# Kernel tuning notes

Hardware: AMD Instinct MI355X
Metric: run time of the kernel (lower is better)

Reference implementation:

```python
import jax, jax.numpy as jnp
import numpy as np

N, H, W, DIM = 8, 32, 32, 768
HEAD_DIM = 64
NUM_HEADS = DIM // HEAD_DIM
KERNEL = (7, 7)
ROT_DIM = HEAD_DIM // 2  # 32
POS_DIM = 2
THETA = 10000.0
LN_EPS = 1e-5


def setup_inputs() -> dict:
    key = jax.random.key(0)
    k_x, k_qkv, k_out = jax.random.split(key, 3)
    S = H * W
    x = jax.random.normal(k_x, (N, S, DIM), dtype=jnp.float32)
    # 2D grid positions, same for every batch element
    grid = jnp.stack(jnp.meshgrid(jnp.arange(H), jnp.arange(W), indexing='ij'), axis=-1)
    pos = jnp.broadcast_to(grid.reshape(1, S, 2), (N, S, 2)).astype(jnp.int32)
    padding_mask = jnp.ones((N, S), dtype=bool)
    ln_g = jnp.ones((DIM,), dtype=jnp.float32)
    ln_b = jnp.zeros((DIM,), dtype=jnp.float32)
    w_qkv = jax.random.normal(k_qkv, (DIM, 3 * DIM), dtype=jnp.float32) * 0.02
    b_qkv = jnp.zeros((3 * DIM,), dtype=jnp.float32)
    w_out = jax.random.normal(k_out, (DIM, DIM), dtype=jnp.float32) * 0.02
    b_out = jnp.zeros((DIM,), dtype=jnp.float32)
    return {"x": x, "pos": pos, "padding_mask": padding_mask,
            "ln_g": ln_g, "ln_b": ln_b,
            "w_qkv": w_qkv, "b_qkv": b_qkv,
            "w_out": w_out, "b_out": b_out}


def _rope_cos_sin(pos):
    # freqs: theta ** linspace(0, -1, rot_dim // (pos_dim*2) + 1)[:-1] -> 8 freqs
    n_freq = ROT_DIM // (POS_DIM * 2)
    freqs = THETA ** jnp.linspace(0.0, -1.0, n_freq + 1, dtype=jnp.float32)[:-1]
    # pos: [n, s, 2] -> [n, s, 2, n_freq] -> [n, s, 2*n_freq] -> [n, 1, s, 2*n_freq]
    tmp = (pos[..., None].astype(jnp.float32) * freqs).reshape(*pos.shape[:-1], -1)[:, None]
    return jnp.cos(tmp), jnp.sin(tmp)


def _apply_rotary(x, cos, sin):
    d = cos.shape[-1]  # 16
    x1, x2, x3 = x[..., :d], x[..., d:2 * d], x[..., 2 * d:]
    y1 = x1 * cos - x2 * sin
    y2 = x2 * cos + x1 * sin
    return jnp.concatenate((y1.astype(x3.dtype), y2.astype(x3.dtype), x3), axis=-1)


def _attn_mask(pos, padding_mask, kernel_size):
    dh = pos[:, :, None, 0] - pos[:, None, :, 0]  # [n, s, s]
    dw = pos[:, :, None, 1] - pos[:, None, :, 1]
    kh, kw = kernel_size
    m = ((dh <= kh // 2) & (dh > -((kh + 1) // 2))
         & (dw <= kw // 2) & (dw > -((kw + 1) // 2)))
    m = m & (padding_mask[:, None, :] & padding_mask[:, :, None])
    return m[:, None]  # [n, 1, s, s]


def reference(x, pos, padding_mask, ln_g, ln_b, w_qkv, b_qkv, w_out, b_out):
    n, s, dim = x.shape
    skip = x
    # LayerNorm
    mu = jnp.mean(x, axis=-1, keepdims=True)
    var = jnp.mean(jnp.square(x - mu), axis=-1, keepdims=True)
    xn = (x - mu) * jax.lax.rsqrt(var + LN_EPS) * ln_g + ln_b
    # QKV projection; split 'n s (t h d)'
    qkv = xn @ w_qkv + b_qkv                       # [n, s, 3*dim]
    qkv = qkv.reshape(n, s, 3, NUM_HEADS, HEAD_DIM)
    qkv = jnp.transpose(qkv, (2, 0, 3, 1, 4))      # [3, n, h, s, d]
    q, k, v = qkv[0], qkv[1], qkv[2]
    # RoPE on first half of head dim
    cos, sin = _rope_cos_sin(pos)
    q = _apply_rotary(q, cos, sin)
    k = _apply_rotary(k, cos, sin)
    # Local 2D-window masked SDPA
    mask = _attn_mask(pos, padding_mask, KERNEL)   # [n, 1, s, s]
    scale = 1.0 / jnp.sqrt(jnp.asarray(HEAD_DIM, dtype=q.dtype))
    scores = jnp.einsum('nhqd,nhkd->nhqk', q, k) * scale
    scores = jnp.where(mask, scores, jnp.asarray(-1e30, dtype=scores.dtype))
    attn = jax.nn.softmax(scores, axis=-1)
    o = jnp.einsum('nhqk,nhkd->nhqd', attn, v)     # [n, h, s, d]
    o = jnp.transpose(o, (0, 2, 1, 3)).reshape(n, s, dim)
    return o @ w_out + b_out + skip
```

## Files before the change

### kernel.cpp

```cpp
#include <hip/hip_runtime.h>


typedef unsigned short u16;
typedef unsigned int   u32;
typedef __attribute__((ext_vector_type(8))) short v8s;
typedef __attribute__((ext_vector_type(4))) float v4f;
typedef __attribute__((ext_vector_type(4))) unsigned short v4us;

#define MFMA16(a,b,c) __builtin_amdgcn_mfma_f32_16x16x32_bf16((a),(b),(c),0,0,0)

__device__ __forceinline__ u16 f2bf(float f){
  union { float f; u32 u; } v; v.f = f;
  u32 u = v.u;
  u32 r = u + 0x7FFFu + ((u >> 16) & 1u);
  return (u16)(r >> 16);
}
__device__ __forceinline__ float bf2f(u16 h){
  union { u32 u; float f; } v; v.u = ((u32)h) << 16;
  return v.f;
}
__device__ __forceinline__ void gll16(const void* g, void* l){
  __builtin_amdgcn_global_load_lds((const __attribute__((address_space(1))) void*)g,
                                   (__attribute__((address_space(3))) void*)l, 16, 0, 0);
}
__device__ __forceinline__ v8s ld8(const u16* p){ return *(const v8s*)p; }
__device__ __forceinline__ void st8(u16* p, v8s v){ *(v8s*)p = v; }

__global__ __launch_bounds__(256) void jet_transpose(const float* __restrict__ in,
                                                     u16* __restrict__ out, int R, int C){
  __shared__ float tile[32][33];
  const int bx = blockIdx.x << 5, by = blockIdx.y << 5;
  const int tx = threadIdx.x & 31, ty = threadIdx.x >> 5;
  #pragma unroll
  for (int i = 0; i < 32; i += 8)
    tile[ty + i][tx] = in[(size_t)(by + ty + i) * C + bx + tx];
  __syncthreads();
  #pragma unroll
  for (int i = 0; i < 32; i += 8)
    out[(size_t)(bx + ty + i) * R + by + tx] = f2bf(tile[tx][ty + i]);
}

__global__ __launch_bounds__(256) void jet_ln(const float* __restrict__ x,
                                              const float* __restrict__ g,
                                              const float* __restrict__ b,
                                              u16* __restrict__ xn){
  const int row = blockIdx.x;
  const int t = threadIdx.x;
  const float* xr = x + (size_t)row * 768;
  float a0 = xr[t], a1 = xr[t + 256], a2 = xr[t + 512];
  float s  = a0 + a1 + a2;
  float ss = a0*a0 + a1*a1 + a2*a2;
  #pragma unroll
  for (int o = 1; o < 64; o <<= 1){ s += __shfl_xor(s, o); ss += __shfl_xor(ss, o); }
  __shared__ float red[8];
  const int wv = t >> 6, lane = t & 63;
  if (lane == 0){ red[wv] = s; red[4 + wv] = ss; }
  __syncthreads();
  s  = red[0] + red[1] + red[2] + red[3];
  ss = red[4] + red[5] + red[6] + red[7];
  const float mu = s * (1.0f / 768.0f);
  const float var = ss * (1.0f / 768.0f) - mu * mu;
  const float rs = rsqrtf(var + 1e-5f);
  u16* o = xn + (size_t)row * 768;
  o[t]       = f2bf((a0 - mu) * rs * g[t]       + b[t]);
  o[t + 256] = f2bf((a1 - mu) * rs * g[t + 256] + b[t + 256]);
  o[t + 512] = f2bf((a2 - mu) * rs * g[t + 512] + b[t + 512]);
}

template<int MODE>
__global__ __launch_bounds__(256, 4)
void jet_gemm(const u16* __restrict__ A, const u16* __restrict__ Bt,
              const float* __restrict__ bias, int K,
              u16* __restrict__ qbuf, u16* __restrict__ kbuf, u16* __restrict__ vbuf,
              const float* __restrict__ skip, float* __restrict__ outp)
{
  __shared__ u16 As[2][128 * 32];
  __shared__ u16 Bs[2][128 * 32];
  const int tid = threadIdx.x;
  const int lane = tid & 63, wv = tid >> 6;
  const int wm = wv >> 1, wn = wv & 1;
  const int row0 = blockIdx.x * 128, col0 = blockIdx.y * 128;
  const int lq = lane & 15, lk = lane >> 4;

  v4f acc[4][4] = {};

  auto stage = [&](int bsel, int kt){
    const int k0 = kt * 32;
    #pragma unroll
    for (int i = 0; i < 2; ++i){
      const int lin = i * 256 + tid;
      const int r = lin >> 2, c = lin & 3;
      const int sc = c ^ ((r >> 1) & 3);
      gll16(A  + (size_t)(row0 + r) * K + k0 + (sc << 3), (void*)&As[bsel][lin << 3]);
      gll16(Bt + (size_t)(col0 + r) * K + k0 + (sc << 3), (void*)&Bs[bsel][lin << 3]);
    }
  };

  stage(0, 0);
  __syncthreads();
  const int KT = K >> 5;
  for (int kt = 0; kt < KT; ++kt){
    const int cur = kt & 1;
    if (kt + 1 < KT) stage(cur ^ 1, kt + 1);
    v8s af[4], bf[4];
    #pragma unroll
    for (int m = 0; m < 4; ++m){
      const int row_ = wm*64 + m*16 + lq;
      af[m] = ld8(&As[cur][row_*32 + ((lk ^ ((row_ >> 1) & 3)) << 3)]);
    }
    #pragma unroll
    for (int n = 0; n < 4; ++n){
      const int row_ = wn*64 + n*16 + lq;
      bf[n] = ld8(&Bs[cur][row_*32 + ((lk ^ ((row_ >> 1) & 3)) << 3)]);
    }
    #pragma unroll
    for (int m = 0; m < 4; ++m)
      #pragma unroll
      for (int n = 0; n < 4; ++n)
        acc[m][n] = MFMA16(af[m], bf[n], acc[m][n]);
    __syncthreads();
  }

  if (MODE == 0){
    const int colw = col0 + wn * 64;
    const int which = colw / 768;
    const int cm = colw - which * 768;
    const int hh = cm >> 6;
    float bb[4];
    #pragma unroll
    for (int n = 0; n < 4; ++n) bb[n] = bias[colw + n * 16 + lq];

    if (which == 2){
      #pragma unroll
      for (int m = 0; m < 4; ++m){
        const int rbase = row0 + wm * 64 + m * 16 + lk * 4;
        const int img = rbase >> 10, s = rbase & 1023;
        u16* vp = vbuf + (size_t)(img * 12 + hh) * 64 * 1024;
        #pragma unroll
        for (int n = 0; n < 4; ++n){
          const int d = n * 16 + lq;
          v4us pk;
          #pragma unroll
          for (int r = 0; r < 4; ++r) pk[r] = f2bf(acc[m][n][r] + bb[n]);
          *(v4us*)&vp[(size_t)d * 1024 + s] = pk;
        }
      }
    } else {
      u16* dst0 = (which == 0) ? qbuf : kbuf;
      const float freq = __expf(-(float)(lq & 7) * 1.1512925464970229f);
      #pragma unroll
      for (int m = 0; m < 4; ++m){
        const int rbase = row0 + wm * 64 + m * 16 + lk * 4;
        const int img = rbase >> 10, sb = rbase & 1023;
        u16* dst = dst0 + ((size_t)(img * 12 + hh) * 1024 + sb) * 64;
        #pragma unroll
        for (int r = 0; r < 4; ++r){
          const int s = sb + r;
          const float coord = (float)((lq < 8) ? (s >> 5) : (s & 31));
          float sn, cs;
          __sincosf(coord * freq, &sn, &cs);
          const float x1 = acc[m][0][r] + bb[0];
          const float x2 = acc[m][1][r] + bb[1];
          u16* dr = dst + (size_t)r * 64;
          dr[lq]      = f2bf(x1 * cs - x2 * sn);
          dr[16 + lq] = f2bf(x2 * cs + x1 * sn);
          dr[32 + lq] = f2bf(acc[m][2][r] + bb[2]);
          dr[48 + lq] = f2bf(acc[m][3][r] + bb[3]);
        }
      }
    }
  } else {
    #pragma unroll
    for (int m = 0; m < 4; ++m){
      const int rbase = row0 + wm*64 + m*16 + lk*4;
      #pragma unroll
      for (int n = 0; n < 4; ++n){
        const int col = col0 + wn*64 + n*16 + lq;
        const float bb = bias[col];
        const size_t o = (size_t)rbase * 768 + col;
        #pragma unroll
        for (int r = 0; r < 4; ++r)
          outp[o + (size_t)r * 768] = acc[m][n][r] + bb + skip[o + (size_t)r * 768];
      }
    }
  }
}

__global__ __launch_bounds__(256, 4)
void jet_attn(const u16* __restrict__ qbuf, const u16* __restrict__ kbuf,
              const u16* __restrict__ vbuf, u16* __restrict__ obuf)
{
  __shared__ u16  Ps[32][232];
  __shared__ float red_m[2][2][16];
  __shared__ float red_s[2][2][16];
  __shared__ u16  Os[32][72];

  const int blk0 = blockIdx.x;
  const int blk = (blk0 & 7) * 384 + (blk0 >> 3);
  const int qh = blk & 31;
  const int nh = blk >> 5;
  const int img = nh / 12, hd = nh - img * 12;
  int h0 = qh - 3; h0 = h0 < 0 ? 0 : (h0 > 25 ? 25 : h0);
  const int s0q = qh * 32, s0k = h0 * 32;
  const int tid = threadIdx.x;
  const int lane = tid & 63, wv = tid >> 6;
  const int lq = lane & 15, lk = lane >> 4;
  const int qg = wv & 1, kh = wv >> 1;

  const u16* kg = kbuf + ((size_t)nh * 1024 + s0k) * 64;
  const u16* vg = vbuf + (size_t)nh * 64 * 1024;

  const u16* qrow = qbuf + ((size_t)nh * 1024 + s0q + qg * 16 + lq) * 64;
  const v8s qf0 = ld8(qrow + lk * 8);
  const v8s qf1 = ld8(qrow + 32 + lk * 8);

  float sc[28];
  const int qw = qg * 16 + lq;
  #pragma unroll
  for (int t = 0; t < 7; ++t){
    const int tile = kh * 7 + t;
    const u16* krow = kg + (size_t)(tile * 16 + lq) * 64;
    const v8s kf0 = ld8(krow + lk * 8);
    const v8s kf1 = ld8(krow + 32 + lk * 8);
    v4f s = {0.f, 0.f, 0.f, 0.f};
    s = MFMA16(kf0, qf0, s);
    s = MFMA16(kf1, qf1, s);
    #pragma unroll
    for (int r = 0; r < 4; ++r){
      const int k = tile * 16 + lk * 4 + r;
      const int dh = qh - (h0 + (k >> 5));
      const int dw = qw - (k & 31);
      const bool ok = (dh <= 3) & (dh >= -3) & (dw <= 3) & (dw >= -3);
      sc[t * 4 + r] = ok ? s[r] * 0.125f : -1e30f;
    }
  }

  float mx = -1e30f;
  #pragma unroll
  for (int i = 0; i < 28; ++i) mx = fmaxf(mx, sc[i]);
  mx = fmaxf(mx, __shfl_xor(mx, 16));
  mx = fmaxf(mx, __shfl_xor(mx, 32));
  if (lk == 0) red_m[qg][kh][lq] = mx;
  __syncthreads();
  const float m_all = fmaxf(mx, red_m[qg][kh ^ 1][lq]);

  float sum = 0.f;
  #pragma unroll
  for (int i = 0; i < 28; ++i){
    const float e = __expf(sc[i] - m_all);
    sc[i] = e; sum += e;
  }
  #pragma unroll
  for (int t = 0; t < 7; ++t){
    v4us pk;
    #pragma unroll
    for (int r = 0; r < 4; ++r) pk[r] = f2bf(sc[t * 4 + r]);
    *(v4us*)&Ps[qw][kh * 112 + t * 16 + lk * 4] = pk;
  }
  sum += __shfl_xor(sum, 16);
  sum += __shfl_xor(sum, 32);
  if (lk == 0) red_s[qg][kh][lq] = sum;
  __syncthreads();

  const int qg2 = wv & 1, dh2 = wv >> 1;
  v4f acc0 = {0.f, 0.f, 0.f, 0.f}, acc1 = {0.f, 0.f, 0.f, 0.f};
  #pragma unroll
  for (int ks = 0; ks < 7; ++ks){
    const v8s af = ld8(&Ps[qg2 * 16 + lq][ks * 32 + lk * 8]);
    const v8s b0 = ld8(vg + (size_t)(dh2 * 32 + lq) * 1024 + s0k + ks * 32 + lk * 8);
    const v8s b1 = ld8(vg + (size_t)(dh2 * 32 + 16 + lq) * 1024 + s0k + ks * 32 + lk * 8);
    acc0 = MFMA16(af, b0, acc0);
    acc1 = MFMA16(af, b1, acc1);
  }
  {
    const int qi = lk * 4;
    #pragma unroll
    for (int r = 0; r < 4; ++r){
      const float inv = 1.0f / (red_s[qg2][0][qi + r] + red_s[qg2][1][qi + r]);
      Os[qg2 * 16 + qi + r][dh2 * 32 + lq]      = f2bf(acc0[r] * inv);
      Os[qg2 * 16 + qi + r][dh2 * 32 + 16 + lq] = f2bf(acc1[r] * inv);
    }
  }
  __syncthreads();
  {
    const int r = tid >> 3, c = (tid & 7) * 8;
    u16* dst = obuf + ((size_t)img * 1024 + s0q + r) * 768 + hd * 64 + c;
    st8(dst, ld8(&Os[r][c]));
  }
}

extern "C" void kernel_launch(void* const* d_in, const int* in_sizes, int n_in,
                              void* d_out, int out_size, void* d_ws, size_t ws_size,
                              hipStream_t stream)
{
  const float* x     = (const float*)d_in[0];
  const float* ln_g  = (const float*)d_in[3];
  const float* ln_b  = (const float*)d_in[4];
  const float* w_qkv = (const float*)d_in[5];
  const float* b_qkv = (const float*)d_in[6];
  const float* w_out = (const float*)d_in[7];
  const float* b_out = (const float*)d_in[8];
  float* out = (float*)d_out;

  char* ws = (char*)d_ws;
  size_t off = 0;
  auto alloc = [&](size_t n){ size_t o = off; off += (n + 255) & ~(size_t)255; return o; };
  u16* xn    = (u16*)(ws + alloc(8192ull * 768 * 2));
  u16* wqkvT = (u16*)(ws + alloc(2304ull * 768 * 2));
  u16* woutT = (u16*)(ws + alloc(768ull  * 768 * 2));
  u16* q_buf = (u16*)(ws + alloc(96ull * 1024 * 64 * 2));
  u16* k_buf = (u16*)(ws + alloc(96ull * 1024 * 64 * 2));
  u16* v_buf = (u16*)(ws + alloc(96ull * 1024 * 64 * 2));
  u16* o_buf = (u16*)(ws + alloc(8192ull * 768 * 2));

  jet_transpose<<<dim3(2304 / 32, 768 / 32), 256, 0, stream>>>(w_qkv, wqkvT, 768, 2304);
  jet_transpose<<<dim3(768 / 32, 768 / 32),  256, 0, stream>>>(w_out, woutT, 768, 768);
  jet_ln<<<8192, 256, 0, stream>>>(x, ln_g, ln_b, xn);
  jet_gemm<0><<<dim3(64, 18), 256, 0, stream>>>(xn, wqkvT, b_qkv, 768,
                                                q_buf, k_buf, v_buf, nullptr, nullptr);
  jet_attn<<<8 * 12 * 32, 256, 0, stream>>>(q_buf, k_buf, v_buf, o_buf);
  jet_gemm<1><<<dim3(64, 6), 256, 0, stream>>>(o_buf, woutT, b_out, 768,
                                               nullptr, nullptr, nullptr, x, out);
}
```

Baseline: 135.5 us.

## Triple-buffer GEMM loads, swizzle block order, fuse weight transposes

The GEMM kernel moves from a double-buffered to a triple-buffered LDS pipeline. It prefetches two K-tiles ahead and replaces __syncthreads with explicit vmcnt waits plus s_barrier, so global loads overlap more MFMA work. Block indices are remapped through a swizzle, placing consecutive blocks on different rows to improve L2 reuse. The two weight-transpose launches are merged into one 3D-grid launch to save a launch. The larger LDS footprint lowers the occupancy hint from 4 to 3 blocks, and the hand-written waitcnt values must match the number of loads each thread issues per stage.

```diff
diff --git a/kernel.cpp b/kernel.cpp
--- a/kernel.cpp
+++ b/kernel.cpp
@@ -26,9 +26,15 @@
 __device__ __forceinline__ v8s ld8(const u16* p){ return *(const v8s*)p; }
 __device__ __forceinline__ void st8(u16* p, v8s v){ *(v8s*)p = v; }
 
-__global__ __launch_bounds__(256) void jet_transpose(const float* __restrict__ in,
-                                                     u16* __restrict__ out, int R, int C){
+__global__ __launch_bounds__(256) void jet_transpose2(const float* __restrict__ in0,
+                                                      u16* __restrict__ out0,
+                                                      const float* __restrict__ in1,
+                                                      u16* __restrict__ out1){
   __shared__ float tile[32][33];
+  const float* in; u16* out; int C;
+  if (blockIdx.z == 0){ in = in0; out = out0; C = 2304; }
+  else { if (blockIdx.x >= 24) return; in = in1; out = out1; C = 768; }
+  const int R = 768;
   const int bx = blockIdx.x << 5, by = blockIdx.y << 5;
   const int tx = threadIdx.x & 31, ty = threadIdx.x >> 5;
   #pragma unroll
@@ -68,19 +74,24 @@
 }
 
 template<int MODE>
-__global__ __launch_bounds__(256, 4)
+__global__ __launch_bounds__(256, 3)
 void jet_gemm(const u16* __restrict__ A, const u16* __restrict__ Bt,
               const float* __restrict__ bias, int K,
               u16* __restrict__ qbuf, u16* __restrict__ kbuf, u16* __restrict__ vbuf,
               const float* __restrict__ skip, float* __restrict__ outp)
 {
-  __shared__ u16 As[2][128 * 32];
-  __shared__ u16 Bs[2][128 * 32];
+  __shared__ u16 As[3][128 * 32];
+  __shared__ u16 Bs[3][128 * 32];
   const int tid = threadIdx.x;
   const int lane = tid & 63, wv = tid >> 6;
   const int wm = wv >> 1, wn = wv & 1;
-  const int row0 = blockIdx.x * 128, col0 = blockIdx.y * 128;
   const int lq = lane & 15, lk = lane >> 4;
+
+  constexpr int NB = (MODE == 0) ? 18 : 6;
+  const int bid = blockIdx.x;
+  const int swz = (bid & 7) * (8 * NB) + (bid >> 3);
+  const int bm = swz / NB, bn = swz - bm * NB;
+  const int row0 = bm * 128, col0 = bn * 128;
 
   v4f acc[4][4] = {};
 
@@ -97,11 +108,15 @@
   };
 
   stage(0, 0);
-  __syncthreads();
+  stage(1, 1);
+  asm volatile("s_waitcnt vmcnt(4)" ::: "memory");
+  asm volatile("s_barrier" ::: "memory");
+
   const int KT = K >> 5;
   for (int kt = 0; kt < KT; ++kt){
-    const int cur = kt & 1;
-    if (kt + 1 < KT) stage(cur ^ 1, kt + 1);
+    const int cur = kt % 3;
+    const bool more = (kt + 2 < KT);
+    if (more) stage((kt + 2) % 3, kt + 2);
     v8s af[4], bf[4];
     #pragma unroll
     for (int m = 0; m < 4; ++m){
@@ -118,7 +133,9 @@
       #pragma unroll
       for (int n = 0; n < 4; ++n)
         acc[m][n] = MFMA16(af[m], bf[n], acc[m][n]);
-    __syncthreads();
+    if (more) asm volatile("s_waitcnt vmcnt(4) lgkmcnt(0)" ::: "memory");
+    else      asm volatile("s_waitcnt vmcnt(0) lgkmcnt(0)" ::: "memory");
+    asm volatile("s_barrier" ::: "memory");
   }
 
   if (MODE == 0){
@@ -313,12 +330,11 @@
   u16* v_buf = (u16*)(ws + alloc(96ull * 1024 * 64 * 2));
   u16* o_buf = (u16*)(ws + alloc(8192ull * 768 * 2));
 
-  jet_transpose<<<dim3(2304 / 32, 768 / 32), 256, 0, stream>>>(w_qkv, wqkvT, 768, 2304);
-  jet_transpose<<<dim3(768 / 32, 768 / 32),  256, 0, stream>>>(w_out, woutT, 768, 768);
+  jet_transpose2<<<dim3(72, 24, 2), 256, 0, stream>>>(w_qkv, wqkvT, w_out, woutT);
   jet_ln<<<8192, 256, 0, stream>>>(x, ln_g, ln_b, xn);
-  jet_gemm<0><<<dim3(64, 18), 256, 0, stream>>>(xn, wqkvT, b_qkv, 768,
-                                                q_buf, k_buf, v_buf, nullptr, nullptr);
+  jet_gemm<0><<<64 * 18, 256, 0, stream>>>(xn, wqkvT, b_qkv, 768,
+                                           q_buf, k_buf, v_buf, nullptr, nullptr);
   jet_attn<<<8 * 12 * 32, 256, 0, stream>>>(q_buf, k_buf, v_buf, o_buf);
-  jet_gemm<1><<<dim3(64, 6), 256, 0, stream>>>(o_buf, woutT, b_out, 768,
-                                               nullptr, nullptr, nullptr, x, out);
-}
+  jet_gemm<1><<<64 * 6, 256, 0, stream>>>(o_buf, woutT, b_out, 768,
+                                          nullptr, nullptr, nullptr, x, out);
+}
```

Measured after the change: 133.6 us. Within noise of the previous version (-1.4%).

## Merge prep kernels into one launch and split attention into single-wave blocks

Applied to the files above, without the earlier changes.

The two weight transposes and the LayerNorm are combined into one launch whose block index selects the work, which removes two launch gaps. Attention now runs one 64-thread wave per 16-query half-row. Each wave covers all 14 key tiles, so the cross-wave max and sum reductions, their __syncthreads barriers and the shared-memory output staging all go away. Normalization is applied to P before the PV matmul. The cost is doubled register use per wave for scores (56 floats), smaller blocks, and uncoalesced scalar 2-byte output stores in place of staged 16-byte stores.

```diff
diff --git a/kernel.cpp b/kernel.cpp
--- a/kernel.cpp
+++ b/kernel.cpp
@@ -26,45 +26,51 @@
 __device__ __forceinline__ v8s ld8(const u16* p){ return *(const v8s*)p; }
 __device__ __forceinline__ void st8(u16* p, v8s v){ *(v8s*)p = v; }
 
-__global__ __launch_bounds__(256) void jet_transpose(const float* __restrict__ in,
-                                                     u16* __restrict__ out, int R, int C){
-  __shared__ float tile[32][33];
-  const int bx = blockIdx.x << 5, by = blockIdx.y << 5;
-  const int tx = threadIdx.x & 31, ty = threadIdx.x >> 5;
-  #pragma unroll
-  for (int i = 0; i < 32; i += 8)
-    tile[ty + i][tx] = in[(size_t)(by + ty + i) * C + bx + tx];
-  __syncthreads();
-  #pragma unroll
-  for (int i = 0; i < 32; i += 8)
-    out[(size_t)(bx + ty + i) * R + by + tx] = f2bf(tile[tx][ty + i]);
-}
-
-__global__ __launch_bounds__(256) void jet_ln(const float* __restrict__ x,
-                                              const float* __restrict__ g,
-                                              const float* __restrict__ b,
-                                              u16* __restrict__ xn){
-  const int row = blockIdx.x;
-  const int t = threadIdx.x;
-  const float* xr = x + (size_t)row * 768;
-  float a0 = xr[t], a1 = xr[t + 256], a2 = xr[t + 512];
-  float s  = a0 + a1 + a2;
-  float ss = a0*a0 + a1*a1 + a2*a2;
-  #pragma unroll
-  for (int o = 1; o < 64; o <<= 1){ s += __shfl_xor(s, o); ss += __shfl_xor(ss, o); }
-  __shared__ float red[8];
-  const int wv = t >> 6, lane = t & 63;
-  if (lane == 0){ red[wv] = s; red[4 + wv] = ss; }
-  __syncthreads();
-  s  = red[0] + red[1] + red[2] + red[3];
-  ss = red[4] + red[5] + red[6] + red[7];
-  const float mu = s * (1.0f / 768.0f);
-  const float var = ss * (1.0f / 768.0f) - mu * mu;
-  const float rs = rsqrtf(var + 1e-5f);
-  u16* o = xn + (size_t)row * 768;
-  o[t]       = f2bf((a0 - mu) * rs * g[t]       + b[t]);
-  o[t + 256] = f2bf((a1 - mu) * rs * g[t + 256] + b[t + 256]);
-  o[t + 512] = f2bf((a2 - mu) * rs * g[t + 512] + b[t + 512]);
+__global__ __launch_bounds__(256)
+void jet_prep(const float* __restrict__ x, const float* __restrict__ g,
+              const float* __restrict__ b, u16* __restrict__ xn,
+              const float* __restrict__ w0, u16* __restrict__ t0,
+              const float* __restrict__ w1, u16* __restrict__ t1)
+{
+  __shared__ float sh[32 * 33];
+  const int bid = blockIdx.x, t = threadIdx.x;
+  if (bid < 8192){
+    const float* xr = x + (size_t)bid * 768;
+    float a0 = xr[t], a1 = xr[t + 256], a2 = xr[t + 512];
+    float s  = a0 + a1 + a2;
+    float ss = a0*a0 + a1*a1 + a2*a2;
+    #pragma unroll
+    for (int o = 1; o < 64; o <<= 1){ s += __shfl_xor(s, o); ss += __shfl_xor(ss, o); }
+    const int wv = t >> 6, lane = t & 63;
+    if (lane == 0){ sh[wv] = s; sh[4 + wv] = ss; }
+    __syncthreads();
+    s  = sh[0] + sh[1] + sh[2] + sh[3];
+    ss = sh[4] + sh[5] + sh[6] + sh[7];
+    const float mu = s * (1.0f / 768.0f);
+    const float var = ss * (1.0f / 768.0f) - mu * mu;
+    const float rs = rsqrtf(var + 1e-5f);
+    u16* o = xn + (size_t)bid * 768;
+    o[t]       = f2bf((a0 - mu) * rs * g[t]       + b[t]);
+    o[t + 256] = f2bf((a1 - mu) * rs * g[t + 256] + b[t + 256]);
+    o[t + 512] = f2bf((a2 - mu) * rs * g[t + 512] + b[t + 512]);
+  } else {
+    const float* in; u16* out; int C, bx, by;
+    if (bid < 8192 + 1728){
+      const int tb = bid - 8192; in = w0; out = t0; C = 2304; bx = tb % 72; by = tb / 72;
+    } else {
+      const int tb = bid - 8192 - 1728; in = w1; out = t1; C = 768; bx = tb % 24; by = tb / 24;
+    }
+    float (*tile)[33] = (float(*)[33])sh;
+    const int x0 = bx << 5, y0 = by << 5;
+    const int tx = t & 31, ty = t >> 5;
+    #pragma unroll
+    for (int i = 0; i < 32; i += 8)
+      tile[ty + i][tx] = in[(size_t)(y0 + ty + i) * C + x0 + tx];
+    __syncthreads();
+    #pragma unroll
+    for (int i = 0; i < 32; i += 8)
+      out[(size_t)(x0 + ty + i) * 768 + y0 + tx] = f2bf(tile[tx][ty + i]);
+  }
 }
 
 template<int MODE>
@@ -186,40 +192,35 @@
   }
 }
 
-__global__ __launch_bounds__(256, 4)
+__global__ __launch_bounds__(64, 4)
 void jet_attn(const u16* __restrict__ qbuf, const u16* __restrict__ kbuf,
               const u16* __restrict__ vbuf, u16* __restrict__ obuf)
 {
-  __shared__ u16  Ps[32][232];
-  __shared__ float red_m[2][2][16];
-  __shared__ float red_s[2][2][16];
-  __shared__ u16  Os[32][72];
-
-  const int blk0 = blockIdx.x;
-  const int blk = (blk0 & 7) * 384 + (blk0 >> 3);
-  const int qh = blk & 31;
-  const int nh = blk >> 5;
+  __shared__ u16 Ps[16][232];
+
+  const int b0 = blockIdx.x;
+  const int blk = (b0 & 7) * 768 + (b0 >> 3);
+  const int half = blk & 1;
+  const int qh = (blk >> 1) & 31;
+  const int nh = blk >> 6;
   const int img = nh / 12, hd = nh - img * 12;
   int h0 = qh - 3; h0 = h0 < 0 ? 0 : (h0 > 25 ? 25 : h0);
-  const int s0q = qh * 32, s0k = h0 * 32;
-  const int tid = threadIdx.x;
-  const int lane = tid & 63, wv = tid >> 6;
+  const int s0k = h0 * 32;
+  const int lane = threadIdx.x;
   const int lq = lane & 15, lk = lane >> 4;
-  const int qg = wv & 1, kh = wv >> 1;
 
   const u16* kg = kbuf + ((size_t)nh * 1024 + s0k) * 64;
   const u16* vg = vbuf + (size_t)nh * 64 * 1024;
 
-  const u16* qrow = qbuf + ((size_t)nh * 1024 + s0q + qg * 16 + lq) * 64;
+  const u16* qrow = qbuf + ((size_t)nh * 1024 + qh * 32 + half * 16 + lq) * 64;
   const v8s qf0 = ld8(qrow + lk * 8);
   const v8s qf1 = ld8(qrow + 32 + lk * 8);
 
-  float sc[28];
-  const int qw = qg * 16 + lq;
-  #pragma unroll
-  for (int t = 0; t < 7; ++t){
-    const int tile = kh * 7 + t;
-    const u16* krow = kg + (size_t)(tile * 16 + lq) * 64;
+  float sc[56];
+  const int qw = half * 16 + lq;
+  #pragma unroll
+  for (int tt = 0; tt < 14; ++tt){
+    const u16* krow = kg + (size_t)(tt * 16 + lq) * 64;
     const v8s kf0 = ld8(krow + lk * 8);
     const v8s kf1 = ld8(krow + 32 + lk * 8);
     v4f s = {0.f, 0.f, 0.f, 0.f};
@@ -227,66 +228,54 @@
     s = MFMA16(kf1, qf1, s);
     #pragma unroll
     for (int r = 0; r < 4; ++r){
-      const int k = tile * 16 + lk * 4 + r;
+      const int k = tt * 16 + lk * 4 + r;
       const int dh = qh - (h0 + (k >> 5));
       const int dw = qw - (k & 31);
       const bool ok = (dh <= 3) & (dh >= -3) & (dw <= 3) & (dw >= -3);
-      sc[t * 4 + r] = ok ? s[r] * 0.125f : -1e30f;
+      sc[tt * 4 + r] = ok ? s[r] * 0.125f : -1e30f;
     }
   }
 
   float mx = -1e30f;
   #pragma unroll
-  for (int i = 0; i < 28; ++i) mx = fmaxf(mx, sc[i]);
+  for (int i = 0; i < 56; ++i) mx = fmaxf(mx, sc[i]);
   mx = fmaxf(mx, __shfl_xor(mx, 16));
   mx = fmaxf(mx, __shfl_xor(mx, 32));
-  if (lk == 0) red_m[qg][kh][lq] = mx;
-  __syncthreads();
-  const float m_all = fmaxf(mx, red_m[qg][kh ^ 1][lq]);
-
   float sum = 0.f;
   #pragma unroll
-  for (int i = 0; i < 28; ++i){
-    const float e = __expf(sc[i] - m_all);
+  for (int i = 0; i < 56; ++i){
+    const float e = __expf(sc[i] - mx);
     sc[i] = e; sum += e;
-  }
-  #pragma unroll
-  for (int t = 0; t < 7; ++t){
-    v4us pk;
-    #pragma unroll
-    for (int r = 0; r < 4; ++r) pk[r] = f2bf(sc[t * 4 + r]);
-    *(v4us*)&Ps[qw][kh * 112 + t * 16 + lk * 4] = pk;
   }
   sum += __shfl_xor(sum, 16);
   sum += __shfl_xor(sum, 32);
-  if (lk == 0) red_s[qg][kh][lq] = sum;
-  __syncthreads();
-
-  const int qg2 = wv & 1, dh2 = wv >> 1;
-  v4f acc0 = {0.f, 0.f, 0.f, 0.f}, acc1 = {0.f, 0.f, 0.f, 0.f};
+  const float inv = 1.0f / sum;
+
+  #pragma unroll
+  for (int tt = 0; tt < 14; ++tt){
+    v4us pk;
+    #pragma unroll
+    for (int r = 0; r < 4; ++r) pk[r] = f2bf(sc[tt * 4 + r] * inv);
+    *(v4us*)&Ps[lq][tt * 16 + lk * 4] = pk;
+  }
+
+  v4f acc[4] = {};
   #pragma unroll
   for (int ks = 0; ks < 7; ++ks){
-    const v8s af = ld8(&Ps[qg2 * 16 + lq][ks * 32 + lk * 8]);
-    const v8s b0 = ld8(vg + (size_t)(dh2 * 32 + lq) * 1024 + s0k + ks * 32 + lk * 8);
-    const v8s b1 = ld8(vg + (size_t)(dh2 * 32 + 16 + lq) * 1024 + s0k + ks * 32 + lk * 8);
-    acc0 = MFMA16(af, b0, acc0);
-    acc1 = MFMA16(af, b1, acc1);
-  }
-  {
-    const int qi = lk * 4;
-    #pragma unroll
-    for (int r = 0; r < 4; ++r){
-      const float inv = 1.0f / (red_s[qg2][0][qi + r] + red_s[qg2][1][qi + r]);
-      Os[qg2 * 16 + qi + r][dh2 * 32 + lq]      = f2bf(acc0[r] * inv);
-      Os[qg2 * 16 + qi + r][dh2 * 32 + 16 + lq] = f2bf(acc1[r] * inv);
-    }
-  }
-  __syncthreads();
-  {
-    const int r = tid >> 3, c = (tid & 7) * 8;
-    u16* dst = obuf + ((size_t)img * 1024 + s0q + r) * 768 + hd * 64 + c;
-    st8(dst, ld8(&Os[r][c]));
-  }
+    const v8s af = ld8(&Ps[lq][ks * 32 + lk * 8]);
+    #pragma unroll
+    for (int n = 0; n < 4; ++n){
+      const v8s bf = ld8(vg + (size_t)(n * 16 + lq) * 1024 + s0k + ks * 32 + lk * 8);
+      acc[n] = MFMA16(af, bf, acc[n]);
+    }
+  }
+
+  u16* dst = obuf + ((size_t)img * 1024 + qh * 32 + half * 16) * 768 + hd * 64;
+  #pragma unroll
+  for (int n = 0; n < 4; ++n)
+    #pragma unroll
+    for (int r = 0; r < 4; ++r)
+      dst[(size_t)(lk * 4 + r) * 768 + n * 16 + lq] = f2bf(acc[n][r]);
 }
 
 extern "C" void kernel_launch(void* const* d_in, const int* in_sizes, int n_in,
@@ -313,12 +302,10 @@
   u16* v_buf = (u16*)(ws + alloc(96ull * 1024 * 64 * 2));
   u16* o_buf = (u16*)(ws + alloc(8192ull * 768 * 2));
 
-  jet_transpose<<<dim3(2304 / 32, 768 / 32), 256, 0, stream>>>(w_qkv, wqkvT, 768, 2304);
-  jet_transpose<<<dim3(768 / 32, 768 / 32),  256, 0, stream>>>(w_out, woutT, 768, 768);
-  jet_ln<<<8192, 256, 0, stream>>>(x, ln_g, ln_b, xn);
+  jet_prep<<<8192 + 1728 + 576, 256, 0, stream>>>(x, ln_g, ln_b, xn, w_qkv, wqkvT, w_out, woutT);
   jet_gemm<0><<<dim3(64, 18), 256, 0, stream>>>(xn, wqkvT, b_qkv, 768,
                                                 q_buf, k_buf, v_buf, nullptr, nullptr);
-  jet_attn<<<8 * 12 * 32, 256, 0, stream>>>(q_buf, k_buf, v_buf, o_buf);
+  jet_attn<<<6144, 64, 0, stream>>>(q_buf, k_buf, v_buf, o_buf);
   jet_gemm<1><<<dim3(64, 6), 256, 0, stream>>>(o_buf, woutT, b_out, 768,
                                                nullptr, nullptr, nullptr, x, out);
 }
```

Result: faster. 126.7 us (-6.5%).
